# Kernel tuning notes

Measured on AMD Instinct MI355X. Metric: run time of the kernel, lower is better.

Reference implementation:

```python
import jax, jax.numpy as jnp
import numpy as np

EMBED = 2048
HEADS = 16
DFF = 4 * EMBED
EPS = 1e-5


def layernorm(x, g, b):
    mu = jnp.mean(x, axis=-1, keepdims=True)
    var = jnp.var(x, axis=-1, keepdims=True)
    return (x - mu) * jax.lax.rsqrt(var + EPS) * g + b


def setup_inputs() -> dict:
    key = jax.random.key(0)
    ks = jax.random.split(key, 16)
    s = 1.0 / np.sqrt(EMBED)
    sf = 1.0 / np.sqrt(DFF)
    return {
        "x": jax.random.normal(ks[0], (2, 2048, EMBED), jnp.float32),
        "Wq": jax.random.normal(ks[1], (EMBED, EMBED), jnp.float32) * s,
        "bq": jnp.zeros((EMBED,), jnp.float32),
        "Wk": jax.random.normal(ks[2], (EMBED, EMBED), jnp.float32) * s,
        "bk": jnp.zeros((EMBED,), jnp.float32),
        "Wv": jax.random.normal(ks[3], (EMBED, EMBED), jnp.float32) * s,
        "bv": jnp.zeros((EMBED,), jnp.float32),
        "Wo": jax.random.normal(ks[4], (EMBED, EMBED), jnp.float32) * s,
        "bo": jnp.zeros((EMBED,), jnp.float32),
        "g1": jnp.ones((EMBED,), jnp.float32),
        "b1": jnp.zeros((EMBED,), jnp.float32),
        "g2": jnp.ones((EMBED,), jnp.float32),
        "b2": jnp.zeros((EMBED,), jnp.float32),
        "W1": jax.random.normal(ks[5], (EMBED, DFF), jnp.float32) * s,
        "bf1": jnp.zeros((DFF,), jnp.float32),
        "W2": jax.random.normal(ks[6], (DFF, EMBED), jnp.float32) * sf,
        "bf2": jnp.zeros((EMBED,), jnp.float32),
    }


def reference(x, Wq, bq, Wk, bk, Wv, bv, Wo, bo, g1, b1, g2, b2, W1, bf1, W2, bf2):
    B, N, C = x.shape
    H = HEADS
    hd = C // H
    # QKV projections -> [B, H, N, hd]
    def split_heads(t):
        return t.reshape(B, N, H, hd).transpose(0, 2, 1, 3)
    q = split_heads(x @ Wq + bq)
    k = split_heads(x @ Wk + bk)
    v = split_heads(x @ Wv + bv)
    # scores [B, H, N, N]
    attn = jnp.einsum('bhqd,bhkd->bhqk', q, k) / np.sqrt(hd)
    attn = jax.nn.softmax(attn, axis=-1)
    out = jnp.einsum('bhqk,bhkd->bhqd', attn, v)
    out = out.transpose(0, 2, 1, 3).reshape(B, N, C)
    out = out @ Wo + bo
    h = layernorm(x + out, g1, b1)
    ff = jax.nn.gelu(h @ W1 + bf1, approximate=False) @ W2 + bf2
    return layernorm(h + ff, g2, b2)
```

## Files before the change

### kernel.cpp

```cpp
#include <hip/hip_runtime.h>
#include <math.h>

#define EMBED 2048
#define DFF   8192
#define TOK   4096
#define SEQ   2048
#define HEADS 16
#define HD    128
#define LDQ   6144

typedef __attribute__((ext_vector_type(8))) short short8;
typedef __attribute__((ext_vector_type(4))) float f32x4;

__device__ __forceinline__ unsigned short f2bf(float f) {
    unsigned int u = __float_as_uint(f);
    return (unsigned short)((u + 0x7FFFu + ((u >> 16) & 1u)) >> 16);
}
__device__ __forceinline__ float bf2f(unsigned short s) {
    return __uint_as_float(((unsigned int)s) << 16);
}
__device__ __forceinline__ float exp2_fast(float x) {
    return __builtin_amdgcn_exp2f(x);
}

__device__ __forceinline__ void async16(const void* g, void* l) {
    __builtin_amdgcn_global_load_lds((const __attribute__((address_space(1))) void*)g,
                                     (__attribute__((address_space(3))) void*)l, 16, 0, 0);
}

__device__ __forceinline__ float gelu_fast(float v) {
    const float y = 1.5957691216057308f * (v + 0.044715f * v * v * v);
    return v / (1.0f + __expf(-y));
}

template<int MODE>
__global__ __launch_bounds__(256, 2)
void gemm_bf16(const unsigned short* __restrict__ A, const unsigned short* __restrict__ B,
               const float* __restrict__ bias, const void* __restrict__ resid,
               unsigned short* __restrict__ C, int M, int N, int K, int lda)
{
    __shared__ __align__(16) float smemf[8448];
    unsigned short* As = (unsigned short*)smemf;
    unsigned short* Bs = As + 8192;
    float* Cs = smemf;

    const int t = threadIdx.x;
    const int w = t >> 6, l = t & 63;
    const int quad = l >> 4, m16 = l & 15;
    const long bm = (long)blockIdx.y * 128, bn = (long)blockIdx.x * 128;
    const int wr = (w >> 1)*64, wc = (w & 1)*64;

    f32x4 acc[4][4] = {};

    const int srow = w*16 + (l >> 2);
    const int sslot = l & 3;
    const unsigned short* Ag = A + (size_t)bm*lda;
    const unsigned short* Bg = B + (size_t)bn*K;

#pragma unroll
    for (int u = 0; u < 2; ++u) {
        const int row = u*64 + srow;
        const int c = sslot ^ ((row >> 1) & 3);
        async16(Ag + (size_t)row*lda + c*8, &As[u*2048 + w*512]);
        async16(Bg + (size_t)row*K   + c*8, &Bs[u*2048 + w*512]);
    }

    const int iters = K >> 5;
    for (int it = 0; it < iters; ++it) {
        __syncthreads();
        if (it + 1 < iters) {
            const int k0 = (it + 1) << 5;
            const int bo = ((it + 1) & 1) * 4096;
#pragma unroll
            for (int u = 0; u < 2; ++u) {
                const int row = u*64 + srow;
                const int c = sslot ^ ((row >> 1) & 3);
                async16(Ag + (size_t)row*lda + k0 + c*8, &As[bo + u*2048 + w*512]);
                async16(Bg + (size_t)row*K   + k0 + c*8, &Bs[bo + u*2048 + w*512]);
            }
        }
        const int co = (it & 1) * 4096;
        short8 af[4], bf[4];
#pragma unroll
        for (int s = 0; s < 4; ++s) {
            const int ra = wr + s*16 + m16;
            const int sla = quad ^ ((ra >> 1) & 3);
            af[s] = *(const short8*)&As[co + ra*32 + sla*8];
            const int rb = wc + s*16 + m16;
            const int slb = quad ^ ((rb >> 1) & 3);
            bf[s] = *(const short8*)&Bs[co + rb*32 + slb*8];
        }
#pragma unroll
        for (int ms = 0; ms < 4; ++ms)
#pragma unroll
            for (int ns = 0; ns < 4; ++ns)
                acc[ms][ns] = __builtin_amdgcn_mfma_f32_16x16x32_bf16(af[ms], bf[ns], acc[ms][ns], 0, 0, 0);
    }

    const int ecol = (t & 15) * 8;
    float bias8[8];
#pragma unroll
    for (int i = 0; i < 8; ++i) bias8[i] = bias[bn + ecol + i];

#pragma unroll
    for (int pass = 0; pass < 2; ++pass) {
        __syncthreads();
        if ((w >> 1) == pass) {
#pragma unroll
            for (int ms = 0; ms < 4; ++ms)
#pragma unroll
                for (int ns = 0; ns < 4; ++ns)
#pragma unroll
                    for (int r = 0; r < 4; ++r)
                        Cs[(ms*16 + quad*4 + r)*132 + wc + ns*16 + m16] = acc[ms][ns][r];
        }
        __syncthreads();
#pragma unroll
        for (int j = 0; j < 4; ++j) {
            const int row = j*16 + (t >> 4);
            float v[8];
            *(f32x4*)&v[0] = *(const f32x4*)&Cs[row*132 + ecol];
            *(f32x4*)&v[4] = *(const f32x4*)&Cs[row*132 + ecol + 4];
            const long gr = bm + pass*64 + row;
            const long go = gr*N + bn + ecol;
            float r8[8];
            if (MODE == 1) {
                *(f32x4*)&r8[0] = *(const f32x4*)((const float*)resid + go);
                *(f32x4*)&r8[4] = *(const f32x4*)((const float*)resid + go + 4);
            }
            short8 rb16;
            if (MODE == 3) rb16 = *(const short8*)((const unsigned short*)resid + go);
            short8 o;
#pragma unroll
            for (int i = 0; i < 8; ++i) {
                float y = v[i] + bias8[i];
                if (MODE == 1) y += r8[i];
                if (MODE == 3) y += bf2f((unsigned short)rb16[i]);
                if (MODE == 2) y = gelu_fast(y);
                o[i] = (short)f2bf(y);
            }
            *(short8*)&C[go] = o;
        }
    }
}

__global__ __launch_bounds__(256, 2)
void attn_flash(unsigned short* __restrict__ qkv)
{
    __shared__ unsigned short Ks2[2][64*128];
    __shared__ unsigned short Vt2[2][128*72];
    __shared__ unsigned short Ps[4*16*72];

    const int t = threadIdx.x;
    const int w = t >> 6, l = t & 63;
    const int quad = l >> 4, m16 = l & 15;

    const int dd = blockIdx.x;
    const int bh = (dd & 7)*4 + ((dd >> 3) >> 4);
    const int qt = (dd >> 3) & 15;
    const int b = bh >> 4, h = bh & 15;

    const long rowq = (long)b*SEQ + qt*128;
    const long rowb = (long)b*SEQ;
    const int qc = h*HD;
    const int kc = EMBED + h*HD;
    const int vc = 2*EMBED + h*HD;

    const int rbase = w*4 + (l >> 4);
    const int slot  = l & 15;
    const int vslot = t & 15;
    const int vrp   = t >> 4;

    unsigned short* QsOv = (unsigned short*)Vt2;

    short8 va[2], vb[2];
#pragma unroll
    for (int u = 0; u < 2; ++u) {
        const int rp = u*16 + vrp;
        va[u] = *(const short8*)(qkv + (rowb + 2*rp    )*LDQ + vc + vslot*8);
        vb[u] = *(const short8*)(qkv + (rowb + 2*rp + 1)*LDQ + vc + vslot*8);
    }
#pragma unroll
    for (int u = 0; u < 8; ++u) {
        const int row = u*16 + rbase;
        const int c = slot ^ ((row >> 1) & 7);
        async16(qkv + (rowq + row)*LDQ + qc + c*8, QsOv + u*2048 + w*512);
    }
#pragma unroll
    for (int u = 0; u < 4; ++u) {
        const int row = u*16 + rbase;
        const int c = slot ^ ((row >> 1) & 7);
        async16(qkv + (rowb + row)*LDQ + kc + c*8, &Ks2[0][u*2048 + w*512]);
    }
    __syncthreads();

    short8 af[2][4];
#pragma unroll
    for (int qh = 0; qh < 2; ++qh)
#pragma unroll
        for (int ks = 0; ks < 4; ++ks) {
            const int row = w*32 + qh*16 + m16;
            const int sl = (4*ks + quad) ^ ((row >> 1) & 7);
            af[qh][ks] = *(const short8*)&QsOv[row*128 + sl*8];
        }
    __syncthreads();

#pragma unroll
    for (int u = 0; u < 2; ++u) {
        const int rp = u*16 + vrp;
#pragma unroll
        for (int i = 0; i < 8; ++i) {
            const int dv = vslot*8 + i;
            const int col = (2*rp) ^ (((dv >> 5) & 3) << 3);
            unsigned int pv = (unsigned int)(unsigned short)va[u][i] |
                              ((unsigned int)(unsigned short)vb[u][i] << 16);
            *(unsigned int*)&Vt2[0][dv*72 + col] = pv;
        }
    }
    __syncthreads();

    f32x4 O[2][8] = {};
    float mrun[2][4], lrun[2][4];
#pragma unroll
    for (int qh = 0; qh < 2; ++qh)
#pragma unroll
        for (int r = 0; r < 4; ++r) { mrun[qh][r] = -1e30f; lrun[qh][r] = 0.f; }
    unsigned short* Pw = Ps + w*16*72;
    const float SC = 0.08838834764831845f * 1.4426950408889634f;

    for (int kt = 0; kt < SEQ/64; ++kt) {
        const int cur = kt & 1;
        const bool pre = (kt + 1 < SEQ/64);
        const long rowkv = rowb + (long)(kt + 1)*64;

        if (pre) {
#pragma unroll
            for (int u = 0; u < 2; ++u) {
                const int rp = u*16 + vrp;
                va[u] = *(const short8*)(qkv + (rowkv + 2*rp    )*LDQ + vc + vslot*8);
                vb[u] = *(const short8*)(qkv + (rowkv + 2*rp + 1)*LDQ + vc + vslot*8);
            }
#pragma unroll
            for (int u = 0; u < 4; ++u) {
                const int row = u*16 + rbase;
                const int c = slot ^ ((row >> 1) & 7);
                async16(qkv + (rowkv + row)*LDQ + kc + c*8, &Ks2[cur^1][u*2048 + w*512]);
            }
        }

        f32x4 S[2][4];
#pragma unroll
        for (int ns = 0; ns < 4; ++ns) {
            f32x4 a0 = {0.f,0.f,0.f,0.f}, a1 = {0.f,0.f,0.f,0.f};
            const int row = ns*16 + m16;
            const int swr = (row >> 1) & 7;
#pragma unroll
            for (int ks = 0; ks < 4; ++ks) {
                const int sl = (4*ks + quad) ^ swr;
                const short8 bfr = *(const short8*)&Ks2[cur][row*128 + sl*8];
                a0 = __builtin_amdgcn_mfma_f32_16x16x32_bf16(af[0][ks], bfr, a0, 0, 0, 0);
                a1 = __builtin_amdgcn_mfma_f32_16x16x32_bf16(af[1][ks], bfr, a1, 0, 0, 0);
            }
#pragma unroll
            for (int r = 0; r < 4; ++r) { a0[r] *= SC; a1[r] *= SC; }
            S[0][ns] = a0; S[1][ns] = a1;
        }

#pragma unroll
        for (int qh = 0; qh < 2; ++qh) {
            float al[4], rs4[4];
#pragma unroll
            for (int r = 0; r < 4; ++r) {
                float tm = fmaxf(fmaxf(S[qh][0][r], S[qh][1][r]), fmaxf(S[qh][2][r], S[qh][3][r]));
                tm = fmaxf(tm, __shfl_xor(tm, 1));
                tm = fmaxf(tm, __shfl_xor(tm, 2));
                tm = fmaxf(tm, __shfl_xor(tm, 4));
                tm = fmaxf(tm, __shfl_xor(tm, 8));
                const float mn = fmaxf(mrun[qh][r], tm);
                al[r] = exp2_fast(mrun[qh][r] - mn);
                mrun[qh][r] = mn;
                rs4[r] = 0.f;
            }
#pragma unroll
            for (int ns = 0; ns < 4; ++ns)
#pragma unroll
                for (int r = 0; r < 4; ++r) {
                    const float p = exp2_fast(S[qh][ns][r] - mrun[qh][r]);
                    rs4[r] += p;
                    Pw[(quad*4 + r)*72 + ns*16 + m16] = f2bf(p);
                }
#pragma unroll
            for (int r = 0; r < 4; ++r) {
                rs4[r] += __shfl_xor(rs4[r], 1);
                rs4[r] += __shfl_xor(rs4[r], 2);
                rs4[r] += __shfl_xor(rs4[r], 4);
                rs4[r] += __shfl_xor(rs4[r], 8);
                lrun[qh][r] = lrun[qh][r]*al[r] + rs4[r];
            }
            if (__any((al[0] != 1.f) | (al[1] != 1.f) | (al[2] != 1.f) | (al[3] != 1.f))) {
#pragma unroll
                for (int i = 0; i < 8; ++i)
#pragma unroll
                    for (int r = 0; r < 4; ++r) O[qh][i][r] *= al[r];
            }

            if (qh == 1 && pre) {
#pragma unroll
                for (int u = 0; u < 2; ++u) {
                    const int rp = u*16 + vrp;
#pragma unroll
                    for (int i = 0; i < 8; ++i) {
                        const int dv = vslot*8 + i;
                        const int col = (2*rp) ^ (((dv >> 5) & 3) << 3);
                        unsigned int pv = (unsigned int)(unsigned short)va[u][i] |
                                          ((unsigned int)(unsigned short)vb[u][i] << 16);
                        *(unsigned int*)&Vt2[cur^1][dv*72 + col] = pv;
                    }
                }
            }

#pragma unroll
            for (int ks2 = 0; ks2 < 2; ++ks2) {
                const short8 ap = *(const short8*)&Pw[m16*72 + ks2*32 + quad*8];
#pragma unroll
                for (int ds = 0; ds < 8; ++ds) {
                    const int dv = ds*16 + m16;
                    const int jcol = (ks2*32 + quad*8) ^ (((dv >> 5) & 3) << 3);
                    const short8 bv = *(const short8*)&Vt2[cur][dv*72 + jcol];
                    O[qh][ds] = __builtin_amdgcn_mfma_f32_16x16x32_bf16(ap, bv, O[qh][ds], 0, 0, 0);
                }
            }
        }

        __syncthreads();
    }

    float inv[2][4];
#pragma unroll
    for (int qh = 0; qh < 2; ++qh)
#pragma unroll
        for (int r = 0; r < 4; ++r) inv[qh][r] = 1.0f / lrun[qh][r];
#pragma unroll
    for (int qh = 0; qh < 2; ++qh)
#pragma unroll
        for (int ds = 0; ds < 8; ++ds)
#pragma unroll
            for (int r = 0; r < 4; ++r) {
                const long row = rowq + w*32 + qh*16 + quad*4 + r;
                qkv[row*LDQ + qc + ds*16 + m16] = f2bf(O[qh][ds][r] * inv[qh][r]);
            }
}

template<int OUTF32>
__global__ __launch_bounds__(256)
void ln_bf16(const unsigned short* __restrict__ X, const float* __restrict__ g,
             const float* __restrict__ be, void* __restrict__ Y)
{
    __shared__ float r1[256], r2[256];
    const int t = threadIdx.x;
    const long row = blockIdx.x;
    const unsigned short* x = X + row*EMBED;
    float v[8];
    const short8 xv = *(const short8*)(x + t*8);
    float s = 0.f, s2 = 0.f;
#pragma unroll
    for (int i = 0; i < 8; ++i) {
        v[i] = bf2f((unsigned short)xv[i]);
        s += v[i]; s2 += v[i]*v[i];
    }
    r1[t] = s; r2[t] = s2;
    __syncthreads();
    for (int k = 128; k > 0; k >>= 1) {
        if (t < k) { r1[t] += r1[t+k]; r2[t] += r2[t+k]; }
        __syncthreads();
    }
    const float mu = r1[0] * (1.0f/EMBED);
    const float var = r2[0] * (1.0f/EMBED) - mu*mu;
    const float rstd = rsqrtf(var + 1e-5f);
    if (OUTF32) {
        float* y = (float*)Y + row*EMBED + t*8;
#pragma unroll
        for (int i = 0; i < 8; ++i) y[i] = (v[i]-mu)*rstd*g[t*8+i] + be[t*8+i];
    } else {
        unsigned short* y = (unsigned short*)Y + row*EMBED;
        short8 o;
#pragma unroll
        for (int i = 0; i < 8; ++i) o[i] = (short)f2bf((v[i]-mu)*rstd*g[t*8+i] + be[t*8+i]);
        *(short8*)(y + t*8) = o;
    }
}

__global__ __launch_bounds__(256)
void cvt_transpose(const float* __restrict__ W, unsigned short* __restrict__ Wt, int K, int N)
{
    __shared__ unsigned short T[32][33];
    const int t = threadIdx.x;
    const long n0 = (long)blockIdx.x*32, k0 = (long)blockIdx.y*32;
    {
        const int r = t >> 3, c = (t & 7)*4;
        const float4 vv = *(const float4*)&W[(k0 + r)*N + n0 + c];
        T[r][c+0] = f2bf(vv.x); T[r][c+1] = f2bf(vv.y);
        T[r][c+2] = f2bf(vv.z); T[r][c+3] = f2bf(vv.w);
    }
    __syncthreads();
    const int rn = t >> 3, kk = (t & 7)*4;
    unsigned int p0 = (unsigned int)T[kk+0][rn] | ((unsigned int)T[kk+1][rn] << 16);
    unsigned int p1 = (unsigned int)T[kk+2][rn] | ((unsigned int)T[kk+3][rn] << 16);
    unsigned int* dst = (unsigned int*)&Wt[(n0 + rn)*K + k0 + kk];
    dst[0] = p0; dst[1] = p1;
}

__global__ __launch_bounds__(256)
void cvt_f32_bf16(const float* __restrict__ X, unsigned short* __restrict__ Y, long n)
{
    const long i = ((long)blockIdx.x*256 + threadIdx.x)*8;
    if (i >= n) return;
    const float4 a = *(const float4*)&X[i];
    const float4 b = *(const float4*)&X[i+4];
    short8 o;
    o[0]=(short)f2bf(a.x); o[1]=(short)f2bf(a.y); o[2]=(short)f2bf(a.z); o[3]=(short)f2bf(a.w);
    o[4]=(short)f2bf(b.x); o[5]=(short)f2bf(b.y); o[6]=(short)f2bf(b.z); o[7]=(short)f2bf(b.w);
    *(short8*)&Y[i] = o;
}

__global__ __launch_bounds__(256)
void concat_bias(const float* __restrict__ bq, const float* __restrict__ bk,
                 const float* __restrict__ bv, float* __restrict__ out)
{
    const int i = blockIdx.x*256 + threadIdx.x;
    if (i < 2048) out[i] = bq[i];
    else if (i < 4096) out[i] = bk[i-2048];
    else if (i < 6144) out[i] = bv[i-4096];
}

extern "C" void kernel_launch(void* const* d_in, const int* in_sizes, int n_in,
                              void* d_out, int out_size, void* d_ws, size_t ws_size,
                              hipStream_t stream)
{
    const float* x   = (const float*)d_in[0];
    const float* Wq  = (const float*)d_in[1];
    const float* bq  = (const float*)d_in[2];
    const float* Wk  = (const float*)d_in[3];
    const float* bk  = (const float*)d_in[4];
    const float* Wv  = (const float*)d_in[5];
    const float* bv  = (const float*)d_in[6];
    const float* Wo  = (const float*)d_in[7];
    const float* bo  = (const float*)d_in[8];
    const float* g1  = (const float*)d_in[9];
    const float* b1  = (const float*)d_in[10];
    const float* g2v = (const float*)d_in[11];
    const float* b2v = (const float*)d_in[12];
    const float* W1  = (const float*)d_in[13];
    const float* bf1 = (const float*)d_in[14];
    const float* W2  = (const float*)d_in[15];
    const float* bf2 = (const float*)d_in[16];
    float* out = (float*)d_out;

    char* ws = (char*)d_ws;
    unsigned short* Wqkvt = (unsigned short*)(ws + 0);
    unsigned short* Wot   = (unsigned short*)(ws + 25165824);
    unsigned short* W1t   = (unsigned short*)(ws + 33554432);
    unsigned short* W2t   = (unsigned short*)(ws + 67108864);
    float*          bqkv  = (float*)         (ws + 100663296);
    char* arenaA = ws + 100687872;
    unsigned short* xb   = (unsigned short*)(arenaA);
    unsigned short* qkv  = (unsigned short*)(arenaA + 16777216);
    unsigned short* res1 = (unsigned short*)(arenaA);
    unsigned short* ff   = (unsigned short*)(arenaA);
    unsigned short* hb   = (unsigned short*)(ws + 167796736);
    unsigned short* res2 = (unsigned short*)(ws + 0);

    const dim3 blk(256);

    cvt_transpose<<<dim3(64,64),  blk, 0, stream>>>(Wq, Wqkvt,             2048, 2048);
    cvt_transpose<<<dim3(64,64),  blk, 0, stream>>>(Wk, Wqkvt + 2048*2048, 2048, 2048);
    cvt_transpose<<<dim3(64,64),  blk, 0, stream>>>(Wv, Wqkvt + 2*2048*2048, 2048, 2048);
    cvt_transpose<<<dim3(64,64),  blk, 0, stream>>>(Wo, Wot, 2048, 2048);
    cvt_transpose<<<dim3(256,64), blk, 0, stream>>>(W1, W1t, 2048, 8192);
    cvt_transpose<<<dim3(64,256), blk, 0, stream>>>(W2, W2t, 8192, 2048);
    concat_bias<<<dim3(24), blk, 0, stream>>>(bq, bk, bv, bqkv);
    cvt_f32_bf16<<<dim3(4096), blk, 0, stream>>>(x, xb, (long)TOK*EMBED);

    gemm_bf16<0><<<dim3(48,32), blk, 0, stream>>>(xb, Wqkvt, bqkv, nullptr, qkv, TOK, 6144, 2048, 2048);
    attn_flash<<<dim3(512), blk, 0, stream>>>(qkv);
    gemm_bf16<1><<<dim3(16,32), blk, 0, stream>>>(qkv, Wot, bo, x, res1, TOK, 2048, 2048, 6144);
    ln_bf16<0><<<dim3(4096), blk, 0, stream>>>(res1, g1, b1, hb);
    gemm_bf16<2><<<dim3(64,32), blk, 0, stream>>>(hb, W1t, bf1, nullptr, ff, TOK, 8192, 2048, 2048);
    gemm_bf16<3><<<dim3(16,32), blk, 0, stream>>>(ff, W2t, bf2, hb, res2, TOK, 2048, 8192, 8192);
    ln_bf16<1><<<dim3(4096), blk, 0, stream>>>(res2, g2v, b2v, out);
}
```

Baseline: 929.8 us.

## Add 8-wave large-tile bf16 GEMM with double-buffered async LDS staging

Introduces a new 512-thread GEMM kernel with 128x256 or 256x256 block tiles, double-buffered global-to-LDS async loads with XOR swizzle, explicit vmcnt waits and MFMA priority hints. It replaces the QKV, FFN1 and FFN2 GEMMs. The larger tiles raise arithmetic intensity and cut redundant global traffic, and the pipelining overlaps loads with MFMA. The cost is fewer blocks, which risks poor CU fill on the smaller grids (256 blocks for FFN2), plus higher register and LDS pressure.

```diff
diff --git a/kernel.cpp b/kernel.cpp
--- a/kernel.cpp
+++ b/kernel.cpp
@@ -31,6 +31,143 @@
 __device__ __forceinline__ float gelu_fast(float v) {
     const float y = 1.5957691216057308f * (v + 0.044715f * v * v * v);
     return v / (1.0f + __expf(-y));
+}
+
+template<int BM, int MODE>
+__global__ __launch_bounds__(512, 2)
+void gemm8p(const unsigned short* __restrict__ A, const unsigned short* __restrict__ B,
+            const float* __restrict__ bias, const void* __restrict__ resid,
+            unsigned short* __restrict__ C, int M, int N, int K, int lda)
+{
+    constexpr int ASLICE = BM * 32;
+    constexpr int BSLICE = 256 * 32;
+    constexpr int LA = BM / 128;
+    constexpr int MF = BM / 32;
+    __shared__ __align__(16) unsigned short sm[4*ASLICE + 4*BSLICE];
+
+    const int t = threadIdx.x;
+    const int w = t >> 6, l = t & 63;
+    const int quad = l >> 4, m16 = l & 15;
+    const int wm = w >> 2, wn = w & 3;
+    const long bm = (long)blockIdx.y * BM, bn = (long)blockIdx.x * 256;
+
+    f32x4 acc[MF][4] = {};
+
+    const unsigned short* Ag = A + (size_t)bm*lda;
+    const unsigned short* Bg = B + (size_t)bn*K;
+
+    auto stageA = [&](int buf, int ks, int k0) {
+#pragma unroll
+        for (int p = 0; p < LA; ++p) {
+            const int e = p*512 + t;
+            const int r = e >> 2, s = e & 3;
+            const int gc = k0 + ks*32 + (s ^ ((r >> 1) & 3))*8;
+            async16(Ag + (size_t)r*lda + gc,
+                    sm + buf*2*ASLICE + ks*ASLICE + (p*512 + w*64)*8);
+        }
+    };
+    auto stageB = [&](int buf, int ks, int k0) {
+#pragma unroll
+        for (int p = 0; p < 2; ++p) {
+            const int e = p*512 + t;
+            const int r = e >> 2, s = e & 3;
+            const int gc = k0 + ks*32 + (s ^ ((r >> 1) & 3))*8;
+            async16(Bg + (size_t)r*K + gc,
+                    sm + 4*ASLICE + buf*2*BSLICE + ks*BSLICE + (p*512 + w*64)*8);
+        }
+    };
+
+    stageA(0, 0, 0); stageB(0, 0, 0);
+    stageA(0, 1, 0); stageB(0, 1, 0);
+
+    const int iters = K >> 6;
+    for (int it = 0; it < iters; ++it) {
+        const int cur = it & 1;
+        const bool pre = (it + 1 < iters);
+        const int kn = (it + 1) << 6;
+
+#pragma unroll
+        for (int kk = 0; kk < 2; ++kk) {
+            if (kk == 0 || pre) {
+                if constexpr (BM == 256) asm volatile("s_waitcnt vmcnt(4)" ::: "memory");
+                else                     asm volatile("s_waitcnt vmcnt(3)" ::: "memory");
+            } else {
+                asm volatile("s_waitcnt vmcnt(0)" ::: "memory");
+            }
+            __builtin_amdgcn_s_barrier();
+            if (pre) { stageA(cur ^ 1, kk, kn); stageB(cur ^ 1, kk, kn); }
+
+            const unsigned short* Ab = sm + cur*2*ASLICE + kk*ASLICE;
+            const unsigned short* Bb = sm + 4*ASLICE + cur*2*BSLICE + kk*BSLICE;
+            short8 afr[MF], bfr[4];
+#pragma unroll
+            for (int m = 0; m < MF; ++m) {
+                const int R = wm*(BM/2) + m*16 + m16;
+                const int sl = quad ^ ((R >> 1) & 3);
+                afr[m] = *(const short8*)(Ab + R*32 + sl*8);
+            }
+#pragma unroll
+            for (int n = 0; n < 4; ++n) {
+                const int R = wn*64 + n*16 + m16;
+                const int sl = quad ^ ((R >> 1) & 3);
+                bfr[n] = *(const short8*)(Bb + R*32 + sl*8);
+            }
+            __builtin_amdgcn_s_setprio(1);
+#pragma unroll
+            for (int m = 0; m < MF; ++m)
+#pragma unroll
+                for (int n = 0; n < 4; ++n)
+                    acc[m][n] = __builtin_amdgcn_mfma_f32_16x16x32_bf16(afr[m], bfr[n], acc[m][n], 0, 0, 0);
+            __builtin_amdgcn_s_setprio(0);
+        }
+    }
+
+    __syncthreads();
+    asm volatile("" ::: "memory");
+    float* Cs = (float*)sm;
+    const int ecol = (t & 31) * 8;
+    float bias8[8];
+#pragma unroll
+    for (int i = 0; i < 8; ++i) bias8[i] = bias[bn + ecol + i];
+
+    constexpr int NP = BM / 64;
+#pragma unroll
+    for (int p = 0; p < NP; ++p) {
+        if (p) __syncthreads();
+        constexpr int HW = (NP == 4) ? 2 : 1;
+        const int pwm = p / HW;
+        const int mp = (NP == 4) ? (p & 1)*4 : 0;
+        if (wm == pwm) {
+#pragma unroll
+            for (int mi = 0; mi < 4; ++mi)
+#pragma unroll
+                for (int n = 0; n < 4; ++n)
+#pragma unroll
+                    for (int r = 0; r < 4; ++r)
+                        Cs[(mi*16 + quad*4 + r)*260 + wn*64 + n*16 + m16] = acc[mp + mi][n][r];
+        }
+        __syncthreads();
+#pragma unroll
+        for (int j = 0; j < 4; ++j) {
+            const int row = j*16 + (t >> 5);
+            float v[8];
+            *(f32x4*)&v[0] = *(const f32x4*)&Cs[row*260 + ecol];
+            *(f32x4*)&v[4] = *(const f32x4*)&Cs[row*260 + ecol + 4];
+            const long gr = bm + p*64 + row;
+            const long go = gr*N + bn + ecol;
+            short8 rb16;
+            if (MODE == 3) rb16 = *(const short8*)((const unsigned short*)resid + go);
+            short8 o;
+#pragma unroll
+            for (int i = 0; i < 8; ++i) {
+                float y = v[i] + bias8[i];
+                if (MODE == 3) y += bf2f((unsigned short)rb16[i]);
+                if (MODE == 2) y = gelu_fast(y);
+                o[i] = (short)f2bf(y);
+            }
+            *(short8*)&C[go] = o;
+        }
+    }
 }
 
 template<int MODE>
@@ -471,6 +608,7 @@
     unsigned short* res2 = (unsigned short*)(ws + 0);
 
     const dim3 blk(256);
+    const dim3 blk8(512);
 
     cvt_transpose<<<dim3(64,64),  blk, 0, stream>>>(Wq, Wqkvt,             2048, 2048);
     cvt_transpose<<<dim3(64,64),  blk, 0, stream>>>(Wk, Wqkvt + 2048*2048, 2048, 2048);
@@ -481,11 +619,11 @@
     concat_bias<<<dim3(24), blk, 0, stream>>>(bq, bk, bv, bqkv);
     cvt_f32_bf16<<<dim3(4096), blk, 0, stream>>>(x, xb, (long)TOK*EMBED);
 
-    gemm_bf16<0><<<dim3(48,32), blk, 0, stream>>>(xb, Wqkvt, bqkv, nullptr, qkv, TOK, 6144, 2048, 2048);
+    gemm8p<128,0><<<dim3(24,32), blk8, 0, stream>>>(xb, Wqkvt, bqkv, nullptr, qkv, TOK, 6144, 2048, 2048);
     attn_flash<<<dim3(512), blk, 0, stream>>>(qkv);
     gemm_bf16<1><<<dim3(16,32), blk, 0, stream>>>(qkv, Wot, bo, x, res1, TOK, 2048, 2048, 6144);
     ln_bf16<0><<<dim3(4096), blk, 0, stream>>>(res1, g1, b1, hb);
-    gemm_bf16<2><<<dim3(64,32), blk, 0, stream>>>(hb, W1t, bf1, nullptr, ff, TOK, 8192, 2048, 2048);
-    gemm_bf16<3><<<dim3(16,32), blk, 0, stream>>>(ff, W2t, bf2, hb, res2, TOK, 2048, 8192, 8192);
+    gemm8p<256,2><<<dim3(32,16), blk8, 0, stream>>>(hb, W1t, bf1, nullptr, ff, TOK, 8192, 2048, 2048);
+    gemm8p<128,3><<<dim3(8,32), blk8, 0, stream>>>(ff, W2t, bf2, hb, res2, TOK, 2048, 8192, 8192);
     ln_bf16<1><<<dim3(4096), blk, 0, stream>>>(res2, g2v, b2v, out);
 }
```

After: 912.7 us. Within noise of the previous version (-1.8%).
